# Performance work log

Measured on AMD Instinct MI355X. Metric: run time of the kernel, lower is better.

The kernel has to match this reference:

```python
import jax, jax.numpy as jnp
import numpy as np


def setup_inputs() -> dict:
    key = jax.random.key(0)
    ks = jax.random.split(key, 8)
    B, N, D, H = 8, 512, 64, 64
    user_embeddings = jax.random.normal(ks[0], (B, N, D), dtype=jnp.float32)
    past_lengths = jax.random.randint(ks[1], (B,), 0, N)
    valid_mask = jnp.ones((B, N), dtype=jnp.float32)
    # MLP params: Linear(4D -> H), PReLU (single slope), Linear(H -> 1)
    s1 = 1.0 / np.sqrt(4 * D)
    s2 = 1.0 / np.sqrt(H)
    W1 = jax.random.uniform(ks[2], (H, 4 * D), minval=-s1, maxval=s1, dtype=jnp.float32)
    b1 = jax.random.uniform(ks[3], (H,), minval=-s1, maxval=s1, dtype=jnp.float32)
    prelu_a = jnp.float32(0.25)
    W2 = jax.random.uniform(ks[4], (1, H), minval=-s2, maxval=s2, dtype=jnp.float32)
    b2 = jax.random.uniform(ks[5], (1,), minval=-s2, maxval=s2, dtype=jnp.float32)
    return {"past_lengths": past_lengths, "user_embeddings": user_embeddings,
            "valid_mask": valid_mask, "W1": W1, "b1": b1, "prelu_a": prelu_a,
            "W2": W2, "b2": b2}


def reference(past_lengths, user_embeddings, valid_mask, W1, b1, prelu_a, W2, b2):
    # DIN local activation attention with causal mask.
    # Original math: h = W1 @ concat(Q, K, Q-K, Q*K) + b1 per (q,k) pair.
    # Split W1 into its 4 D-sized blocks so the concat tensor [B,N,N,4D] is
    # never materialized; the pairwise hidden [B,N,N,H] is the only big buffer.
    B, N, D = user_embeddings.shape
    Wq, Wk, Wd, Wm = jnp.split(W1, 4, axis=1)  # each [H, D]
    x = user_embeddings
    # Q and (Q-K)'s +Q part -> per-query term; K and (Q-K)'s -K part -> per-key term
    hq = jnp.einsum('bqd,hd->bqh', x, Wq + Wd)          # [B,N,H]
    hk = jnp.einsum('bkd,hd->bkh', x, Wk - Wd)          # [B,N,H]
    hm = jnp.einsum('bqd,bkd,hd->bqkh', x, x, Wm)       # [B,N,N,H] (Q*K term)
    h = hq[:, :, None, :] + hk[:, None, :, :] + hm + b1
    h = jnp.where(h > 0, h, prelu_a * h)                # PReLU
    scores = jnp.einsum('bqkh,h->bqk', h, W2[0]) + b2[0]  # [B,N,N]
    causal = jnp.tril(jnp.ones((N, N), dtype=scores.dtype))
    scores = scores * causal[None, :, :]
    scores = scores * valid_mask[:, None, :]            # key-side padding mask
    encoded = jnp.einsum('bqk,bkd->bqd', scores, x)     # weighted sum (no softmax)
    return encoded
```

## Files before the change

kernel.cpp:

```cpp
#include <hip/hip_runtime.h>

#define NB 8
#define NN 512

#define WS_WMF 0
#define WS_HQ  4096
#define WS_BF  266240
#define WS_XE  528384
#define WS_WQF 659456

typedef float fx4 __attribute__((ext_vector_type(4)));
typedef short sx8 __attribute__((ext_vector_type(8)));
typedef int   ix4 __attribute__((ext_vector_type(4)));

static __device__ inline unsigned short f2bf(float f) {
    unsigned u = __float_as_uint(f);
    return (unsigned short)((u + 0x7FFFu + ((u >> 16) & 1u)) >> 16);
}

static __device__ inline void async_cp16(const void* g, void* l) {
    __builtin_amdgcn_global_load_lds(
        (const __attribute__((address_space(1))) unsigned int*)g,
        (__attribute__((address_space(3))) unsigned int*)l, 16, 0, 0);
}

__global__ __launch_bounds__(256) void prepW(const float* __restrict__ W1,
                                             float* __restrict__ ws) {
    const int t = threadIdx.x, blk = blockIdx.x;
    unsigned short* wqf = (unsigned short*)(ws + WS_WQF);

    {
        int e = blk * 256 + t;
        int slot = e >> 6, lane = e & 63;
        int isK = slot >> 3, ht = (slot >> 1) & 3, half = slot & 1;
        int n = lane & 15, qd = lane >> 4;
        int h = ht * 16 + n, dbase = half * 32 + qd * 8;
        unsigned short u[8];
        #pragma unroll
        for (int j = 0; j < 8; ++j) {
            int d = dbase + j;
            float wq = W1[h * 256 + d];
            float wk = W1[h * 256 + 64 + d];
            float wd = W1[h * 256 + 128 + d];
            u[j] = f2bf(isK ? (wk - wd) : (wq + wd));
        }
        uint4 o;
        o.x = (unsigned)u[0] | ((unsigned)u[1] << 16);
        o.y = (unsigned)u[2] | ((unsigned)u[3] << 16);
        o.z = (unsigned)u[4] | ((unsigned)u[5] << 16);
        o.w = (unsigned)u[6] | ((unsigned)u[7] << 16);
        ((uint4*)wqf)[e] = o;
    }

    if (blk < 2) {
        float* wmf = ws + WS_WMF;
        int e = blk * 256 + t;
        int slot = e >> 6, lane = e & 63;
        int ht = slot >> 1, hf = slot & 1;
        int m = lane & 15, qd = lane >> 4;
        int h = ht * 16 + m;
        int dbase = hf * 32 + qd * 8;
        #pragma unroll
        for (int j = 0; j < 8; ++j)
            wmf[e * 8 + j] = W1[h * 256 + 192 + dbase + j];
    }
}

__global__ __launch_bounds__(256) void prepX(const float* __restrict__ x,
                                             const float* __restrict__ vm,
                                             const float* __restrict__ b1,
                                             float* __restrict__ ws) {
    const int t = threadIdx.x;
    const int w = t >> 6, lane = t & 63;
    const int n = lane & 15, quad = lane >> 4;
    const int blk = blockIdx.x;
    const int b   = blk >> 3;
    const int tb  = (blk & 7) * 4;
    const int tile = tb + w;

    const unsigned short* wqf = (const unsigned short*)(ws + WS_WQF);
    unsigned short* bfp = (unsigned short*)(ws + WS_BF);
    unsigned short* xep = (unsigned short*)(ws + WS_XE);
    float* hqp = ws + WS_HQ;

    sx8 ax0, ax1;
    {
        const float* xp = x + ((b * 512 + tile * 16 + n) * 64 + quad * 8);
        fx4 a0 = *(const fx4*)xp;
        fx4 a1 = *(const fx4*)(xp + 4);
        fx4 a2 = *(const fx4*)(xp + 32);
        fx4 a3 = *(const fx4*)(xp + 36);
        #pragma unroll
        for (int j = 0; j < 4; ++j) {
            ax0[j] = (short)f2bf(a0[j]); ax0[4 + j] = (short)f2bf(a1[j]);
            ax1[j] = (short)f2bf(a2[j]); ax1[4 + j] = (short)f2bf(a3[j]);
        }
    }

    *(uint4*)(bfp + ((((b * 32 + tile) * 4 + 0) * 64 + lane) << 3)) =
        __builtin_bit_cast(uint4, ax0);
    *(uint4*)(bfp + ((((b * 32 + tile) * 4 + 1) * 64 + lane) << 3)) =
        __builtin_bit_cast(uint4, ax1);

    #pragma unroll
    for (int ht = 0; ht < 4; ++ht) {
        sx8 bq0 = *(const sx8*)(wqf + ((ht * 2 + 0) << 9) + lane * 8);
        sx8 bq1 = *(const sx8*)(wqf + ((ht * 2 + 1) << 9) + lane * 8);
        sx8 bk0 = *(const sx8*)(wqf + ((8 + ht * 2 + 0) << 9) + lane * 8);
        sx8 bk1 = *(const sx8*)(wqf + ((8 + ht * 2 + 1) << 9) + lane * 8);

        float bv = b1[ht * 16 + n];
        fx4 hqa = (fx4){bv, bv, bv, bv};
        hqa = __builtin_amdgcn_mfma_f32_16x16x32_bf16(ax0, bq0, hqa, 0, 0, 0);
        hqa = __builtin_amdgcn_mfma_f32_16x16x32_bf16(ax1, bq1, hqa, 0, 0, 0);
        fx4 hka = (fx4){0.f, 0.f, 0.f, 0.f};
        hka = __builtin_amdgcn_mfma_f32_16x16x32_bf16(ax0, bk0, hka, 0, 0, 0);
        hka = __builtin_amdgcn_mfma_f32_16x16x32_bf16(ax1, bk1, hka, 0, 0, 0);

        #pragma unroll
        for (int r = 0; r < 4; ++r)
            hqp[(b * 512 + tile * 16 + quad * 4 + r) * 64 + ht * 16 + n] = hqa[r];

        int c   = 2 + (ht >> 1);
        int qd2 = (((ht & 1) * 16 + n) >> 3);
        int j   = n & 7;
        #pragma unroll
        for (int r = 0; r < 4; ++r) {
            int nn = quad * 4 + r;
            bfp[((((b * 32 + tile) * 4 + c) * 64 + (qd2 * 16 + nn)) << 3) + j] =
                f2bf(hka[r]);
        }
    }

    #pragma unroll 1
    for (int i = 0; i < 4; ++i) {
        int t5 = tb + i;
        int c32 = t5 >> 1, half = t5 & 1;
        int nt = t >> 6, r = t & 63;
        int L = half * 32 + (r & 31);
        int j0 = (r >> 5) * 4;
        int qd3 = L >> 4, nn3 = L & 15;
        unsigned short u[4];
        #pragma unroll
        for (int ii = 0; ii < 4; ++ii) {
            int key = c32 * 32 + qd3 * 8 + j0 + ii;
            float v = x[(b * 512 + key) * 64 + nt * 16 + nn3] * vm[b * 512 + key];
            u[ii] = f2bf(v);
        }
        uint2 o;
        o.x = (unsigned)u[0] | ((unsigned)u[1] << 16);
        o.y = (unsigned)u[2] | ((unsigned)u[3] << 16);
        *(uint2*)(xep + (((((b * 16 + c32) * 4 + nt) * 64 + L) << 3) + j0)) = o;
    }
}

__global__ __launch_bounds__(256, 2) void k2_main(const float* __restrict__ x,
                                                  const float* __restrict__ prelu_a,
                                                  const float* __restrict__ W2,
                                                  const float* __restrict__ b2,
                                                  const float* __restrict__ ws,
                                                  float* __restrict__ out) {
    const int tid  = threadIdx.x;
    const int lane = tid & 63;
    const int w    = tid >> 6;
    const int blk  = blockIdx.x;
    const int band = (int)((0x4501763298DCABEFULL >> ((blk >> 6) << 2)) & 0xF);
    const int rest = blk & 63;
    const int b    = rest >> 3;
    const int s    = rest & 7;
    const int n    = lane & 15, quad = lane >> 4;
    const int q    = band * 32 + s * 4 + w;
    const int bq   = b * 512 + q;
    const int cmax = band;

    const float* wmf = ws + WS_WMF;
    const float* hq  = ws + WS_HQ;
    const unsigned short* bfp = (const unsigned short*)(ws + WS_BF);
    const unsigned short* xep = (const unsigned short*)(ws + WS_XE);

    const float pa  = prelu_a[0];
    const float b2v = b2[0];

    __shared__ uint4 bufS[2][512];
    __shared__ uint4 bufE[2][256];
    __shared__ unsigned strip[4][16];

    fx4 w2v[4];
    #pragma unroll
    for (int ht = 0; ht < 4; ++ht)
        w2v[ht] = *(const fx4*)(W2 + ht * 16 + quad * 4);
    sx8 oh[4];
    #pragma unroll
    for (int ht = 0; ht < 4; ++ht) {
        sx8 a;
        #pragma unroll
        for (int jj = 0; jj < 8; ++jj) {
            int hp = (ht >> 1) * 32 + quad * 8 + jj;
            a[jj] = (hp == ht * 16 + n) ? (short)0x3F80 : (short)0;
        }
        oh[ht] = a;
    }
    const unsigned sel = (quad < 2) ? 0x05040100u : 0x07060302u;

    fx4 hqv[4];
    #pragma unroll
    for (int ht = 0; ht < 4; ++ht)
        hqv[ht] = *(const fx4*)(hq + bq * 64 + ht * 16 + quad * 4);
    float xq[2][8];
    {
        const float* xp = x + bq * 64 + quad * 8;
        fx4 t0 = *(const fx4*)xp;
        fx4 t1 = *(const fx4*)(xp + 4);
        fx4 t2 = *(const fx4*)(xp + 32);
        fx4 t3 = *(const fx4*)(xp + 36);
        #pragma unroll
        for (int jj = 0; jj < 4; ++jj) {
            xq[0][jj] = t0[jj]; xq[0][4 + jj] = t1[jj];
            xq[1][jj] = t2[jj]; xq[1][4 + jj] = t3[jj];
        }
    }
    sx8 afrag[4][2];
    #pragma unroll
    for (int ht = 0; ht < 4; ++ht)
        #pragma unroll
        for (int hf = 0; hf < 2; ++hf) {
            const float* wp = wmf + (((ht * 2 + hf) * 64 + lane) << 3);
            fx4 w0 = *(const fx4*)wp;
            fx4 w1 = *(const fx4*)(wp + 4);
            sx8 a;
            #pragma unroll
            for (int jj = 0; jj < 4; ++jj) {
                a[jj]     = (short)f2bf(w0[jj] * xq[hf][jj]);
                a[4 + jj] = (short)f2bf(w1[jj] * xq[hf][4 + jj]);
            }
            afrag[ht][hf] = a;
        }

    fx4 eacc[4];
    #pragma unroll
    for (int nt = 0; nt < 4; ++nt) eacc[nt] = (fx4){0.f, 0.f, 0.f, 0.f};

    {
        const uint4* sS = (const uint4*)(bfp + (unsigned)(b * 32) * 2048);
        const uint4* sE = (const uint4*)(xep + (unsigned)(b * 16) * 2048);
        async_cp16(sS + tid,       &bufS[0][tid]);
        async_cp16(sS + tid + 256, &bufS[0][tid + 256]);
        async_cp16(sE + tid,       &bufE[0][tid]);
    }
    __syncthreads();

    #pragma unroll 1
    for (int c = 0; c <= cmax; ++c) {
        if (c < cmax) {
            const int p2 = (c + 1) & 1;
            const uint4* sS = (const uint4*)(bfp + (unsigned)(b * 32 + 2 * (c + 1)) * 2048);
            const uint4* sE = (const uint4*)(xep + (unsigned)(b * 16 + c + 1) * 2048);
            async_cp16(sS + tid,       &bufS[p2][tid]);
            async_cp16(sS + tid + 256, &bufS[p2][tid + 256]);
            async_cp16(sE + tid,       &bufE[p2][tid]);
        }

        const int p = c & 1;
        const unsigned short* ls = (const unsigned short*)&bufS[p][0] + lane * 8;
        sx8 fa0 = *(const sx8*)(ls);
        sx8 fa1 = *(const sx8*)(ls + 512);
        sx8 fa2 = *(const sx8*)(ls + 1024);
        sx8 fa3 = *(const sx8*)(ls + 1536);
        sx8 fb0 = *(const sx8*)(ls + 2048);
        sx8 fb1 = *(const sx8*)(ls + 2560);
        sx8 fb2 = *(const sx8*)(ls + 3072);
        sx8 fb3 = *(const sx8*)(ls + 3584);

        fx4 accA[4], accB[4];
        #pragma unroll
        for (int ht = 0; ht < 4; ++ht) { accA[ht] = hqv[ht]; accB[ht] = hqv[ht]; }
        #pragma unroll
        for (int ht = 0; ht < 4; ++ht) {
            accA[ht] = __builtin_amdgcn_mfma_f32_16x16x32_bf16(afrag[ht][0], fa0, accA[ht], 0, 0, 0);
            accB[ht] = __builtin_amdgcn_mfma_f32_16x16x32_bf16(afrag[ht][0], fb0, accB[ht], 0, 0, 0);
        }
        #pragma unroll
        for (int ht = 0; ht < 4; ++ht) {
            accA[ht] = __builtin_amdgcn_mfma_f32_16x16x32_bf16(afrag[ht][1], fa1, accA[ht], 0, 0, 0);
            accB[ht] = __builtin_amdgcn_mfma_f32_16x16x32_bf16(afrag[ht][1], fb1, accB[ht], 0, 0, 0);
        }
        #pragma unroll
        for (int ht = 0; ht < 4; ++ht) {
            accA[ht] = __builtin_amdgcn_mfma_f32_16x16x32_bf16(oh[ht], (ht < 2) ? fa2 : fa3, accA[ht], 0, 0, 0);
            accB[ht] = __builtin_amdgcn_mfma_f32_16x16x32_bf16(oh[ht], (ht < 2) ? fb2 : fb3, accB[ht], 0, 0, 0);
        }

        fx4 s0v = (fx4){0.f, 0.f, 0.f, 0.f};
        fx4 s1v = (fx4){0.f, 0.f, 0.f, 0.f};
        #pragma unroll
        for (int ht = 0; ht < 4; ++ht) {
            fx4 za = accA[ht], zb = accB[ht];
            fx4 ta = __builtin_elementwise_max(za, za * pa);
            fx4 tb = __builtin_elementwise_max(zb, zb * pa);
            s0v = ta * w2v[ht] + s0v;
            s1v = tb * w2v[ht] + s1v;
        }
        float s0 = (s0v[0] + s0v[1]) + (s0v[2] + s0v[3]);
        float s1 = (s1v[0] + s1v[1]) + (s1v[2] + s1v[3]);
        s0 += __shfl_xor(s0, 16, 64);
        s0 += __shfl_xor(s0, 32, 64);
        s1 += __shfl_xor(s1, 16, 64);
        s1 += __shfl_xor(s1, 32, 64);
        int k0 = c * 32 + n;
        s0 = (k0 <= q)      ? s0 + b2v : 0.f;
        s1 = (k0 + 16 <= q) ? s1 + b2v : 0.f;

        unsigned packed = (unsigned)f2bf(s0) | ((unsigned)f2bf(s1) << 16);
        if (quad == 0) strip[w][n] = packed;
        const unsigned* sp = &strip[w][(quad & 1) * 8];
        uint4 wv0 = *(const uint4*)sp;
        uint4 wv1 = *(const uint4*)(sp + 4);
        ix4 sw_;
        sw_[0] = (int)__builtin_amdgcn_perm(wv0.y, wv0.x, sel);
        sw_[1] = (int)__builtin_amdgcn_perm(wv0.w, wv0.z, sel);
        sw_[2] = (int)__builtin_amdgcn_perm(wv1.y, wv1.x, sel);
        sw_[3] = (int)__builtin_amdgcn_perm(wv1.w, wv1.z, sel);
        sx8 sfrag = __builtin_bit_cast(sx8, sw_);

        const unsigned short* le = (const unsigned short*)&bufE[p][0] + lane * 8;
        sx8 e0 = *(const sx8*)(le);
        sx8 e1 = *(const sx8*)(le + 512);
        sx8 e2 = *(const sx8*)(le + 1024);
        sx8 e3 = *(const sx8*)(le + 1536);

        eacc[0] = __builtin_amdgcn_mfma_f32_16x16x32_bf16(sfrag, e0, eacc[0], 0, 0, 0);
        eacc[1] = __builtin_amdgcn_mfma_f32_16x16x32_bf16(sfrag, e1, eacc[1], 0, 0, 0);
        eacc[2] = __builtin_amdgcn_mfma_f32_16x16x32_bf16(sfrag, e2, eacc[2], 0, 0, 0);
        eacc[3] = __builtin_amdgcn_mfma_f32_16x16x32_bf16(sfrag, e3, eacc[3], 0, 0, 0);

        __syncthreads();
    }

    float ov = eacc[0][0];
    if (quad == 1) ov = eacc[1][0];
    if (quad == 2) ov = eacc[2][0];
    if (quad == 3) ov = eacc[3][0];
    out[bq * 64 + lane] = ov;
}

extern "C" void kernel_launch(void* const* d_in, const int* in_sizes, int n_in,
                              void* d_out, int out_size, void* d_ws, size_t ws_size,
                              hipStream_t stream) {
    const float* x   = (const float*)d_in[1];
    const float* vmk = (const float*)d_in[2];
    const float* W1  = (const float*)d_in[3];
    const float* b1  = (const float*)d_in[4];
    const float* pa  = (const float*)d_in[5];
    const float* W2  = (const float*)d_in[6];
    const float* b2  = (const float*)d_in[7];
    float* ws  = (float*)d_ws;
    float* out = (float*)d_out;

    hipLaunchKernelGGL(prepW, dim3(4), dim3(256), 0, stream, W1, ws);
    hipLaunchKernelGGL(prepX, dim3(64), dim3(256), 0, stream, x, vmk, b1, ws);
    hipLaunchKernelGGL(k2_main, dim3(1024), dim3(256), 0, stream,
                       x, pa, W2, b2, ws, out);
}
```

Before: 102.1 us.

## Fuse weight prep into X prep and rebalance main kernel with split-K waves

Removes the separate prepW launch: each prep block rebuilds the bf16 Wq/Wk fragments in shared memory, trading a kernel launch for redundant weight conversion in every block. The main kernel is restructured so each block pairs a short band with a long band (m and 15-m) to balance causal work. Two waves split the key chunks of each query (even/odd), and their partials are summed through shared memory. The async LDS double-buffering and per-iteration barriers are dropped in favour of direct global (cache-resident) fragment loads. This doubles the grid to more, smaller blocks but loses the explicit prefetch overlap.

```diff
diff --git a/kernel.cpp b/kernel.cpp
--- a/kernel.cpp
+++ b/kernel.cpp
@@ -7,7 +7,6 @@
 #define WS_HQ  4096
 #define WS_BF  266240
 #define WS_XE  528384
-#define WS_WQF 659456
 
 typedef float fx4 __attribute__((ext_vector_type(4)));
 typedef short sx8 __attribute__((ext_vector_type(8)));
@@ -18,58 +17,11 @@
     return (unsigned short)((u + 0x7FFFu + ((u >> 16) & 1u)) >> 16);
 }
 
-static __device__ inline void async_cp16(const void* g, void* l) {
-    __builtin_amdgcn_global_load_lds(
-        (const __attribute__((address_space(1))) unsigned int*)g,
-        (__attribute__((address_space(3))) unsigned int*)l, 16, 0, 0);
-}
-
-__global__ __launch_bounds__(256) void prepW(const float* __restrict__ W1,
-                                             float* __restrict__ ws) {
-    const int t = threadIdx.x, blk = blockIdx.x;
-    unsigned short* wqf = (unsigned short*)(ws + WS_WQF);
-
-    {
-        int e = blk * 256 + t;
-        int slot = e >> 6, lane = e & 63;
-        int isK = slot >> 3, ht = (slot >> 1) & 3, half = slot & 1;
-        int n = lane & 15, qd = lane >> 4;
-        int h = ht * 16 + n, dbase = half * 32 + qd * 8;
-        unsigned short u[8];
-        #pragma unroll
-        for (int j = 0; j < 8; ++j) {
-            int d = dbase + j;
-            float wq = W1[h * 256 + d];
-            float wk = W1[h * 256 + 64 + d];
-            float wd = W1[h * 256 + 128 + d];
-            u[j] = f2bf(isK ? (wk - wd) : (wq + wd));
-        }
-        uint4 o;
-        o.x = (unsigned)u[0] | ((unsigned)u[1] << 16);
-        o.y = (unsigned)u[2] | ((unsigned)u[3] << 16);
-        o.z = (unsigned)u[4] | ((unsigned)u[5] << 16);
-        o.w = (unsigned)u[6] | ((unsigned)u[7] << 16);
-        ((uint4*)wqf)[e] = o;
-    }
-
-    if (blk < 2) {
-        float* wmf = ws + WS_WMF;
-        int e = blk * 256 + t;
-        int slot = e >> 6, lane = e & 63;
-        int ht = slot >> 1, hf = slot & 1;
-        int m = lane & 15, qd = lane >> 4;
-        int h = ht * 16 + m;
-        int dbase = hf * 32 + qd * 8;
-        #pragma unroll
-        for (int j = 0; j < 8; ++j)
-            wmf[e * 8 + j] = W1[h * 256 + 192 + dbase + j];
-    }
-}
-
-__global__ __launch_bounds__(256) void prepX(const float* __restrict__ x,
-                                             const float* __restrict__ vm,
-                                             const float* __restrict__ b1,
-                                             float* __restrict__ ws) {
+__global__ __launch_bounds__(256) void prep(const float* __restrict__ x,
+                                            const float* __restrict__ vm,
+                                            const float* __restrict__ W1,
+                                            const float* __restrict__ b1,
+                                            float* __restrict__ ws) {
     const int t = threadIdx.x;
     const int w = t >> 6, lane = t & 63;
     const int n = lane & 15, quad = lane >> 4;
@@ -78,7 +30,45 @@
     const int tb  = (blk & 7) * 4;
     const int tile = tb + w;
 
-    const unsigned short* wqf = (const unsigned short*)(ws + WS_WQF);
+    __shared__ unsigned short lwf[16 * 64 * 8];
+    #pragma unroll
+    for (int i = 0; i < 4; ++i) {
+        int e = t + i * 256;
+        int slot = e >> 6, L = e & 63;
+        int isK = slot >> 3, ht = (slot >> 1) & 3, half = slot & 1;
+        int nn = L & 15, qd = L >> 4;
+        int h = ht * 16 + nn, dbase = half * 32 + qd * 8;
+        unsigned short u[8];
+        #pragma unroll
+        for (int j = 0; j < 8; ++j) {
+            int d = dbase + j;
+            float wq = W1[h * 256 + d];
+            float wk = W1[h * 256 + 64 + d];
+            float wd = W1[h * 256 + 128 + d];
+            u[j] = f2bf(isK ? (wk - wd) : (wq + wd));
+        }
+        uint4 o;
+        o.x = (unsigned)u[0] | ((unsigned)u[1] << 16);
+        o.y = (unsigned)u[2] | ((unsigned)u[3] << 16);
+        o.z = (unsigned)u[4] | ((unsigned)u[5] << 16);
+        o.w = (unsigned)u[6] | ((unsigned)u[7] << 16);
+        ((uint4*)lwf)[e] = o;
+    }
+
+    if (blk < 2) {
+        float* wmf = ws + WS_WMF;
+        int e = blk * 256 + t;
+        int slot = e >> 6, L = e & 63;
+        int ht = slot >> 1, hf = slot & 1;
+        int m = L & 15, qd = L >> 4;
+        int h = ht * 16 + m;
+        int dbase = hf * 32 + qd * 8;
+        #pragma unroll
+        for (int j = 0; j < 8; ++j)
+            wmf[e * 8 + j] = W1[h * 256 + 192 + dbase + j];
+    }
+    __syncthreads();
+
     unsigned short* bfp = (unsigned short*)(ws + WS_BF);
     unsigned short* xep = (unsigned short*)(ws + WS_XE);
     float* hqp = ws + WS_HQ;
@@ -104,10 +94,10 @@
 
     #pragma unroll
     for (int ht = 0; ht < 4; ++ht) {
-        sx8 bq0 = *(const sx8*)(wqf + ((ht * 2 + 0) << 9) + lane * 8);
-        sx8 bq1 = *(const sx8*)(wqf + ((ht * 2 + 1) << 9) + lane * 8);
-        sx8 bk0 = *(const sx8*)(wqf + ((8 + ht * 2 + 0) << 9) + lane * 8);
-        sx8 bk1 = *(const sx8*)(wqf + ((8 + ht * 2 + 1) << 9) + lane * 8);
+        sx8 bq0 = *(const sx8*)(lwf + ((ht * 2 + 0) << 9) + lane * 8);
+        sx8 bq1 = *(const sx8*)(lwf + ((ht * 2 + 1) << 9) + lane * 8);
+        sx8 bk0 = *(const sx8*)(lwf + ((8 + ht * 2 + 0) << 9) + lane * 8);
+        sx8 bk1 = *(const sx8*)(lwf + ((8 + ht * 2 + 1) << 9) + lane * 8);
 
         float bv = b1[ht * 16 + n];
         fx4 hqa = (fx4){bv, bv, bv, bv};
@@ -154,24 +144,26 @@
     }
 }
 
-__global__ __launch_bounds__(256, 2) void k2_main(const float* __restrict__ x,
-                                                  const float* __restrict__ prelu_a,
-                                                  const float* __restrict__ W2,
-                                                  const float* __restrict__ b2,
-                                                  const float* __restrict__ ws,
-                                                  float* __restrict__ out) {
+__global__ __launch_bounds__(256, 2) void k3(const float* __restrict__ x,
+                                             const float* __restrict__ prelu_a,
+                                             const float* __restrict__ W2,
+                                             const float* __restrict__ b2,
+                                             const float* __restrict__ ws,
+                                             float* __restrict__ out) {
     const int tid  = threadIdx.x;
     const int lane = tid & 63;
     const int w    = tid >> 6;
     const int blk  = blockIdx.x;
-    const int band = (int)((0x4501763298DCABEFULL >> ((blk >> 6) << 2)) & 0xF);
-    const int rest = blk & 63;
-    const int b    = rest >> 3;
-    const int s    = rest & 7;
-    const int n    = lane & 15, quad = lane >> 4;
-    const int q    = band * 32 + s * 4 + w;
+    const int m    = blk >> 8;
+    const int b    = (blk >> 5) & 7;
+    const int s    = blk & 31;
+    const int qsel = w >> 1;
+    const int h    = w & 1;
+    const int band = qsel ? (15 - m) : m;
+    const int q    = band * 32 + s;
     const int bq   = b * 512 + q;
     const int cmax = band;
+    const int n    = lane & 15, quad = lane >> 4;
 
     const float* wmf = ws + WS_WMF;
     const float* hq  = ws + WS_HQ;
@@ -181,9 +173,8 @@
     const float pa  = prelu_a[0];
     const float b2v = b2[0];
 
-    __shared__ uint4 bufS[2][512];
-    __shared__ uint4 bufE[2][256];
     __shared__ unsigned strip[4][16];
+    __shared__ float red[4][64];
 
     fx4 w2v[4];
     #pragma unroll
@@ -240,28 +231,9 @@
     #pragma unroll
     for (int nt = 0; nt < 4; ++nt) eacc[nt] = (fx4){0.f, 0.f, 0.f, 0.f};
 
-    {
-        const uint4* sS = (const uint4*)(bfp + (unsigned)(b * 32) * 2048);
-        const uint4* sE = (const uint4*)(xep + (unsigned)(b * 16) * 2048);
-        async_cp16(sS + tid,       &bufS[0][tid]);
-        async_cp16(sS + tid + 256, &bufS[0][tid + 256]);
-        async_cp16(sE + tid,       &bufE[0][tid]);
-    }
-    __syncthreads();
-
     #pragma unroll 1
-    for (int c = 0; c <= cmax; ++c) {
-        if (c < cmax) {
-            const int p2 = (c + 1) & 1;
-            const uint4* sS = (const uint4*)(bfp + (unsigned)(b * 32 + 2 * (c + 1)) * 2048);
-            const uint4* sE = (const uint4*)(xep + (unsigned)(b * 16 + c + 1) * 2048);
-            async_cp16(sS + tid,       &bufS[p2][tid]);
-            async_cp16(sS + tid + 256, &bufS[p2][tid + 256]);
-            async_cp16(sE + tid,       &bufE[p2][tid]);
-        }
-
-        const int p = c & 1;
-        const unsigned short* ls = (const unsigned short*)&bufS[p][0] + lane * 8;
+    for (int c = h; c <= cmax; c += 2) {
+        const unsigned short* ls = bfp + ((((b * 32 + 2 * c) * 4) * 64 + lane) << 3);
         sx8 fa0 = *(const sx8*)(ls);
         sx8 fa1 = *(const sx8*)(ls + 512);
         sx8 fa2 = *(const sx8*)(ls + 1024);
@@ -270,6 +242,11 @@
         sx8 fb1 = *(const sx8*)(ls + 2560);
         sx8 fb2 = *(const sx8*)(ls + 3072);
         sx8 fb3 = *(const sx8*)(ls + 3584);
+        const unsigned short* le = xep + ((((b * 16 + c) * 4) * 64 + lane) << 3);
+        sx8 e0 = *(const sx8*)(le);
+        sx8 e1 = *(const sx8*)(le + 512);
+        sx8 e2 = *(const sx8*)(le + 1024);
+        sx8 e3 = *(const sx8*)(le + 1536);
 
         fx4 accA[4], accB[4];
         #pragma unroll
@@ -322,25 +299,26 @@
         sw_[3] = (int)__builtin_amdgcn_perm(wv1.w, wv1.z, sel);
         sx8 sfrag = __builtin_bit_cast(sx8, sw_);
 
-        const unsigned short* le = (const unsigned short*)&bufE[p][0] + lane * 8;
-        sx8 e0 = *(const sx8*)(le);
-        sx8 e1 = *(const sx8*)(le + 512);
-        sx8 e2 = *(const sx8*)(le + 1024);
-        sx8 e3 = *(const sx8*)(le + 1536);
-
         eacc[0] = __builtin_amdgcn_mfma_f32_16x16x32_bf16(sfrag, e0, eacc[0], 0, 0, 0);
         eacc[1] = __builtin_amdgcn_mfma_f32_16x16x32_bf16(sfrag, e1, eacc[1], 0, 0, 0);
         eacc[2] = __builtin_amdgcn_mfma_f32_16x16x32_bf16(sfrag, e2, eacc[2], 0, 0, 0);
         eacc[3] = __builtin_amdgcn_mfma_f32_16x16x32_bf16(sfrag, e3, eacc[3], 0, 0, 0);
-
-        __syncthreads();
     }
 
     float ov = eacc[0][0];
     if (quad == 1) ov = eacc[1][0];
     if (quad == 2) ov = eacc[2][0];
     if (quad == 3) ov = eacc[3][0];
-    out[bq * 64 + lane] = ov;
+    red[w][lane] = ov;
+    __syncthreads();
+
+    if (tid < 128) {
+        int qs  = tid >> 6;
+        int d   = tid & 63;
+        int bnd = qs ? (15 - m) : m;
+        int bqo = b * 512 + bnd * 32 + s;
+        out[bqo * 64 + d] = red[qs * 2][d] + red[qs * 2 + 1][d];
+    }
 }
 
 extern "C" void kernel_launch(void* const* d_in, const int* in_sizes, int n_in,
@@ -356,8 +334,7 @@
     float* ws  = (float*)d_ws;
     float* out = (float*)d_out;
 
-    hipLaunchKernelGGL(prepW, dim3(4), dim3(256), 0, stream, W1, ws);
-    hipLaunchKernelGGL(prepX, dim3(64), dim3(256), 0, stream, x, vmk, b1, ws);
-    hipLaunchKernelGGL(k2_main, dim3(1024), dim3(256), 0, stream,
+    hipLaunchKernelGGL(prep, dim3(64), dim3(256), 0, stream, x, vmk, W1, b1, ws);
+    hipLaunchKernelGGL(k3, dim3(2048), dim3(256), 0, stream,
                        x, pa, W2, b2, ws, out);
 }
```

After: 110.2 us. 7.9% more time.
